# Kernel optimization log

Measured on AMD Instinct MI355X. Metric: run time of the kernel, lower is better.

Reference implementation:

```python
import jax, jax.numpy as jnp
import numpy as np

B, L, E, H = 64, 512, 128, 256


def setup_inputs() -> dict:
    key = jax.random.key(0)
    ks = jax.random.split(key, 16)
    s = 0.05
    return {
        "embedded_inputs": jax.random.normal(ks[0], (B, L, E), jnp.float32),
        "decoder_input": jax.random.normal(ks[1], (B, E), jnp.float32),
        "h0": jax.random.normal(ks[2], (B, H), jnp.float32),
        "c0": jax.random.normal(ks[3], (B, H), jnp.float32),
        "context": jax.random.normal(ks[4], (B, L, H), jnp.float32),
        # LSTM cell params
        "Wi": jax.random.normal(ks[5], (4 * H, E), jnp.float32) * s,
        "bi": jnp.zeros((4 * H,), jnp.float32),
        "Wh": jax.random.normal(ks[6], (4 * H, H), jnp.float32) * s,
        "bh": jnp.zeros((4 * H,), jnp.float32),
        # hidden_out: Linear(2H -> H)
        "Wo": jax.random.normal(ks[7], (H, 2 * H), jnp.float32) * s,
        "bo": jnp.zeros((H,), jnp.float32),
        # attention params: input_linear(H->H), context conv1d(H->H,k=1), V [H]
        "Wa_in": jax.random.normal(ks[8], (H, H), jnp.float32) * s,
        "ba_in": jnp.zeros((H,), jnp.float32),
        "Wa_ctx": jax.random.normal(ks[9], (H, H), jnp.float32) * s,
        "ba_ctx": jnp.zeros((H,), jnp.float32),
        "V": jax.random.normal(ks[10], (H,), jnp.float32) * s,
    }


def reference(embedded_inputs, decoder_input, h0, c0, context,
              Wi, bi, Wh, bh, Wo, bo, Wa_in, ba_in, Wa_ctx, ba_ctx, V):
    # Precompute projected context once (Conv1d with kernel 1 == per-position linear): [B,L,H]
    ctx_proj = jnp.einsum('blh,gh->blg', context, Wa_ctx) + ba_ctx

    def step(carry, _):
        dec_in, h, c, mask = carry
        gates = dec_in @ Wi.T + bi + h @ Wh.T + bh              # [B,4H]
        i_g, f_g, g_g, o_g = jnp.split(gates, 4, axis=1)
        i_g = jax.nn.sigmoid(i_g)
        f_g = jax.nn.sigmoid(f_g)
        g_g = jnp.tanh(g_g)
        o_g = jax.nn.sigmoid(o_g)
        c_t = f_g * c + i_g * g_g
        h_t = o_g * jnp.tanh(c_t)
        # attention
        inp = h_t @ Wa_in.T + ba_in                              # [B,H]
        scores = jnp.einsum('h,blh->bl', V, jnp.tanh(inp[:, None, :] + ctx_proj))
        scores = jnp.where(mask == 0, -jnp.inf, scores)
        alpha = jax.nn.softmax(scores, axis=1)                   # [B,L]
        att_hidden = jnp.einsum('bl,blh->bh', alpha, ctx_proj)
        hidden_t = jnp.tanh(jnp.concatenate([att_hidden, h_t], axis=1) @ Wo.T + bo)
        # pointer: argmax over still-available positions
        masked_outs = alpha * mask
        idx = jnp.argmax(masked_outs, axis=1)                    # [B]
        one_hot = jax.nn.one_hot(idx, L, dtype=mask.dtype)
        mask_next = mask * (1.0 - one_hot)
        dec_next = jnp.take_along_axis(embedded_inputs, idx[:, None, None], axis=1)[:, 0]
        return (dec_next, hidden_t, c_t, mask_next), (alpha, idx)

    mask0 = jnp.ones((B, L), jnp.float32)
    carry0 = (decoder_input, h0, c0, mask0)
    (dec_f, h_f, c_f, _), (alphas, ptrs) = jax.lax.scan(step, carry0, None, length=L)
    outputs = jnp.transpose(alphas, (1, 0, 2))                   # [B,L,L]
    pointers = jnp.transpose(ptrs, (1, 0))                       # [B,L]
    return outputs, pointers, h_f, c_f
```

## Files before the change

### kernel.cpp

```cpp
#include <hip/hip_runtime.h>
#include <math.h>

#define SCOPE __HIP_MEMORY_SCOPE_AGENT

constexpr int Bn = 64, Ln = 512, En = 128, Hn = 256, Tn = 512;
constexpr int NBLK = 256, NTHR = 512;
constexpr int CTX_LD = 260, HTPAD = 264, XPAD = 384, UPAD = 520;

constexpr int OFF_CTX = 0;
constexpr int OFF_SCR = 128 * CTX_LD;
constexpr int OFF_HT  = OFF_SCR + 4096;
constexpr int OFF_INP = OFF_HT + 4 * HTPAD;
constexpr int OFF_SS  = OFF_INP + 256;
constexpr int OFF_ES  = OFF_SS + 128;
constexpr int OFF_MK  = OFF_ES + 128;
constexpr int OFF_VS  = OFF_MK + 128;
constexpr int OFF_GS  = OFF_VS + 256;
constexpr int OFF_ST  = OFF_GS + 256;
constexpr int OFF_WR  = OFF_ST + 64;
constexpr int OFF_BA  = OFF_WR + 64;
constexpr int OFF_HTL = OFF_BA + 256;
constexpr int SMEM_FL = OFF_HTL + 64;

constexpr size_t PTR_OFF = (size_t)Bn * Ln * Ln;
constexpr size_t HF_OFF  = PTR_OFF + (size_t)Bn * Ln;
constexpr size_t CF_OFF  = HF_OFF + (size_t)Bn * Hn;

constexpr int GQ_HT    = 0;
constexpr int GQ_HID   = 1024;
constexpr int GQ_ATT   = 2048;
constexpr int GQ_STATS = 6144;
constexpr int GQ_INPP  = 6208;
constexpr int GQ_STRIDE = 6208 + 16384;

__device__ __forceinline__ float fast_tanh(float x) {
  const float e = __expf(2.0f * x);
  return 1.0f - __fdividef(2.0f, 1.0f + e);
}
__device__ __forceinline__ float sigmoidf_(float x) {
  return 1.0f / (1.0f + expf(-x));
}
__device__ __forceinline__ void llc_storef(float* p, float v) {
  __hip_atomic_store(p, v, __ATOMIC_RELAXED, SCOPE);
}
__device__ __forceinline__ float4 llc_ld4(const float* p) {
  float4 r;
  asm volatile("global_load_dwordx4 %0, %1, off sc0 sc1\n\ts_waitcnt vmcnt(0)"
               : "=&v"(r) : "v"(p) : "memory");
  return r;
}
__device__ __forceinline__ void llc_ld4x4(const float* p0, const float* p1,
                                          const float* p2, const float* p3,
                                          float4& a, float4& b, float4& c, float4& d) {
  asm volatile(
      "global_load_dwordx4 %0, %4, off sc0 sc1\n\t"
      "global_load_dwordx4 %1, %5, off sc0 sc1\n\t"
      "global_load_dwordx4 %2, %6, off sc0 sc1\n\t"
      "global_load_dwordx4 %3, %7, off sc0 sc1\n\t"
      "s_waitcnt vmcnt(0)"
      : "=&v"(a), "=&v"(b), "=&v"(c), "=&v"(d)
      : "v"(p0), "v"(p1), "v"(p2), "v"(p3) : "memory");
}

__device__ __forceinline__ void group_barrier16(unsigned* flags_g, int j, unsigned tgt) {
  asm volatile("s_waitcnt vmcnt(0)" ::: "memory");
  __syncthreads();
  if (threadIdx.x == 0)
    __hip_atomic_store(&flags_g[j * 32], tgt, __ATOMIC_RELAXED, SCOPE);
  if (threadIdx.x < 16) {
    long spins = 0;
    while (__hip_atomic_load(&flags_g[threadIdx.x * 32], __ATOMIC_RELAXED, SCOPE) < tgt) {
      __builtin_amdgcn_s_sleep(1);
      if (++spins > 50000000L) __builtin_trap();
    }
  }
  __syncthreads();
  asm volatile("" ::: "memory");
}

#define DOT4(acc, w4, x4) \
  acc = fmaf((w4).x, (x4).x, fmaf((w4).y, (x4).y, fmaf((w4).z, (x4).z, fmaf((w4).w, (x4).w, (acc)))))

__global__ void __launch_bounds__(NTHR, 2)
decoder_main(const float* __restrict__ emb, const float* __restrict__ dec0,
             const float* __restrict__ h0,  const float* __restrict__ c0,
             const float* __restrict__ ctxg,const float* __restrict__ Wi,
             const float* __restrict__ bi,  const float* __restrict__ Wh,
             const float* __restrict__ bh,  const float* __restrict__ Wo,
             const float* __restrict__ bo,  const float* __restrict__ Wain,
             const float* __restrict__ bain,const float* __restrict__ Wactx,
             const float* __restrict__ bactx,const float* __restrict__ Vv,
             float* __restrict__ out, unsigned* __restrict__ flags,
             float* __restrict__ wsd)
{
  extern __shared__ float sm[];
  float* ctx    = sm + OFF_CTX;
  float* scr    = sm + OFF_SCR;
  float* x_s    = sm + OFF_SCR;
  float* h_t_s  = sm + OFF_HT;
  float* inp_s  = sm + OFF_INP;
  float* s_s    = sm + OFF_SS;
  float* e_s    = sm + OFF_ES;
  float* mask_s = sm + OFF_MK;
  float* V_s    = sm + OFF_VS;
  float* gsum   = sm + OFF_GS;
  float* stats_s= sm + OFF_ST;
  float* wred   = sm + OFF_WR;
  float* bain_s = sm + OFF_BA;
  float* htl_s  = sm + OFF_HTL;
  int*   wredi  = (int*)wred;

  const int tid = threadIdx.x, bid = blockIdx.x;
  const int gq = bid >> 4, j = bid & 15;
  const int bbj = j >> 2, ck = j & 3;
  const int b_ctx = gq * 4 + bbj;
  const int l0 = ck * 128;

  const int team = tid >> 3, seg8 = tid & 7;
  const int gteam = team >> 4, hloc = team & 15;
  const int r_abs = gteam * 256 + j * 16 + hloc;
  const int g2 = tid >> 1, half = tid & 1;
  const int r16loc = tid >> 5, seg32 = tid & 31;
  const int r16 = j * 16 + r16loc;

  unsigned* flags_g = flags + gq * (16 * 32);
  float* wsg = wsd + (size_t)gq * GQ_STRIDE;

  float4 wg4[12];
  #pragma unroll
  for (int k = 0; k < 4; ++k) wg4[k] = *(const float4*)&Wi[(size_t)r_abs * En + k * 32 + seg8 * 4];
  #pragma unroll
  for (int k = 0; k < 8; ++k) wg4[4 + k] = *(const float4*)&Wh[(size_t)r_abs * Hn + k * 32 + seg8 * 4];
  const float bias_g = bi[r_abs] + bh[r_abs];

  float4 wa4[2];
  #pragma unroll
  for (int k = 0; k < 2; ++k)
    wa4[k] = *(const float4*)&Wain[(size_t)g2 * Hn + j * 16 + half * 8 + k * 4];

  float4 wo4[4];
  #pragma unroll
  for (int k = 0; k < 4; ++k) wo4[k] = *(const float4*)&Wo[(size_t)r16 * (2 * Hn) + k * 128 + seg32 * 4];
  const float bo_r = bo[r16];

  float cst = 0.0f;
  if (tid < 64) cst = c0[(size_t)(gq * 4 + (tid >> 4)) * Hn + j * 16 + (tid & 15)];

  if (tid < 128) mask_s[tid] = 1.0f;
  if (tid < 256) { V_s[tid] = Vv[tid]; bain_s[tid] = bain[tid]; }

  {
    const int gc = tid & 31, lg = tid >> 5;
    float acc[8][8];
    #pragma unroll
    for (int a2 = 0; a2 < 8; ++a2)
      #pragma unroll
      for (int b2 = 0; b2 < 8; ++b2) acc[a2][b2] = 0.0f;
    float* stg_c = scr;
    float* stg_w = scr + 1024;
    for (int kc = 0; kc < 32; ++kc) {
      __syncthreads();
      for (int i = tid; i < 1024; i += NTHR) {
        int k = i & 7, l = i >> 3;
        stg_c[k * 128 + l] = ctxg[((size_t)(b_ctx * Ln + l0 + l)) * Hn + kc * 8 + k];
      }
      for (int i = tid; i < 2048; i += NTHR) {
        int k = i & 7, gg = i >> 3;
        stg_w[k * 256 + gg] = Wactx[(size_t)gg * Hn + kc * 8 + k];
      }
      __syncthreads();
      #pragma unroll
      for (int kk = 0; kk < 8; ++kk) {
        float cl[8], wgt[8];
        #pragma unroll
        for (int jj = 0; jj < 8; ++jj) cl[jj] = stg_c[kk * 128 + lg * 8 + jj];
        #pragma unroll
        for (int jj = 0; jj < 8; ++jj) wgt[jj] = stg_w[kk * 256 + gc * 8 + jj];
        #pragma unroll
        for (int li = 0; li < 8; ++li)
          #pragma unroll
          for (int gi = 0; gi < 8; ++gi)
            acc[li][gi] = fmaf(cl[li], wgt[gi], acc[li][gi]);
      }
    }
    __syncthreads();
    #pragma unroll
    for (int li = 0; li < 8; ++li)
      #pragma unroll
      for (int gi = 0; gi < 8; ++gi)
        ctx[(lg * 8 + li) * CTX_LD + gc * 8 + gi] = acc[li][gi] + bactx[gc * 8 + gi];
  }
  __syncthreads();

  unsigned tgt = 1;
  int w0 = 0, w1 = 0, w2 = 0, w3 = 0;

  for (int t = 0; t < Tn; ++t) {
    {
      if (tid < 256) {
        const int bbx = tid >> 6, h4 = tid & 63;
        float4 v;
        if (t == 0) v = *(const float4*)&h0[(size_t)(gq * 4 + bbx) * Hn + h4 * 4];
        else        v = llc_ld4(wsg + GQ_HID + bbx * 256 + h4 * 4);
        *(float4*)&x_s[bbx * XPAD + 128 + h4 * 4] = v;
      } else if (tid < 384) {
        const int i2 = tid - 256, bbx = i2 >> 5, k4 = i2 & 31;
        const int gb = gq * 4 + bbx;
        float4 v;
        if (t == 0) v = *(const float4*)&dec0[(size_t)gb * En + k4 * 4];
        else {
          const int wsel = (bbx == 0) ? w0 : (bbx == 1) ? w1 : (bbx == 2) ? w2 : w3;
          v = *(const float4*)&emb[((size_t)gb * Ln + wsel) * En + k4 * 4];
        }
        *(float4*)&x_s[bbx * XPAD + k4 * 4] = v;
      }
      __syncthreads();
      #pragma unroll
      for (int bb = 0; bb < 4; ++bb) {
        float acc = 0.0f;
        #pragma unroll
        for (int k = 0; k < 12; ++k) {
          const float4 x4 = *(const float4*)&x_s[bb * XPAD + k * 32 + seg8 * 4];
          DOT4(acc, wg4[k], x4);
        }
        acc += __shfl_xor(acc, 1, 64);
        acc += __shfl_xor(acc, 2, 64);
        acc += __shfl_xor(acc, 4, 64);
        if (seg8 == 0) gsum[bb * 64 + team] = acc + bias_g;
      }
      __syncthreads();
      if (tid < 64) {
        const int bbx = tid >> 4, hx = tid & 15;
        const float iv = gsum[bbx * 64 + hx];
        const float fv = gsum[bbx * 64 + 16 + hx];
        const float gv = gsum[bbx * 64 + 32 + hx];
        const float ov = gsum[bbx * 64 + 48 + hx];
        const float cn = sigmoidf_(fv) * cst + sigmoidf_(iv) * tanhf(gv);
        const float htv = sigmoidf_(ov) * tanhf(cn);
        cst = cn;
        htl_s[bbx * 16 + hx] = htv;
        llc_storef(wsg + GQ_HT + bbx * 256 + j * 16 + hx, htv);
        if (t == Tn - 1) out[CF_OFF + (size_t)(gq * 4 + bbx) * Hn + j * 16 + hx] = cn;
      }
      __syncthreads();
      {
        float pac[4];
        #pragma unroll
        for (int bb = 0; bb < 4; ++bb) {
          float acc = 0.0f;
          #pragma unroll
          for (int k = 0; k < 2; ++k) {
            const float4 x4 = *(const float4*)&htl_s[bb * 16 + half * 8 + k * 4];
            DOT4(acc, wa4[k], x4);
          }
          pac[bb] = acc;
        }
        #pragma unroll
        for (int bb = 0; bb < 4; ++bb) {
          const float o = __shfl_xor(pac[bb], 1, 64);
          pac[bb] += o;
        }
        if (half == 0) {
          #pragma unroll
          for (int bb = 0; bb < 4; ++bb)
            llc_storef(wsg + GQ_INPP + bb * 4096 + g2 * 16 + j, pac[bb]);
        }
      }
    }
    group_barrier16(flags_g, j, tgt++);

    {
      if (tid < 256) {
        const int bbx = tid >> 6, h4 = tid & 63;
        const float4 v = llc_ld4(wsg + GQ_HT + tid * 4);
        *(float4*)&h_t_s[bbx * HTPAD + h4 * 4] = v;
        const float* ib = wsg + GQ_INPP + bbj * 4096 + tid * 16;
        float4 a0, a1, a2, a3;
        llc_ld4x4(ib, ib + 4, ib + 8, ib + 12, a0, a1, a2, a3);
        const float s01 = ((a0.x + a0.y) + (a0.z + a0.w)) + ((a1.x + a1.y) + (a1.z + a1.w));
        const float s23 = ((a2.x + a2.y) + (a2.z + a2.w)) + ((a3.x + a3.y) + (a3.z + a3.w));
        inp_s[tid] = s01 + s23 + bain_s[tid];
      }
      __syncthreads();
      {
        const int l = tid >> 2, q = tid & 3;
        float p = 0.0f;
        #pragma unroll
        for (int i = 0; i < 16; ++i) {
          const int h4 = q * 64 + i * 4;
          const float4 c4 = *(const float4*)&ctx[l * CTX_LD + h4];
          const float4 in4 = *(const float4*)&inp_s[h4];
          const float4 v4 = *(const float4*)&V_s[h4];
          p = fmaf(v4.x, fast_tanh(in4.x + c4.x), p);
          p = fmaf(v4.y, fast_tanh(in4.y + c4.y), p);
          p = fmaf(v4.z, fast_tanh(in4.z + c4.z), p);
          p = fmaf(v4.w, fast_tanh(in4.w + c4.w), p);
        }
        p += __shfl_xor(p, 1, 64);
        p += __shfl_xor(p, 2, 64);
        if (q == 0) s_s[l] = (mask_s[l] == 0.0f) ? -INFINITY : p;
      }
      __syncthreads();
      if (tid < 128) {
        const float sv = s_s[tid];
        const float e = expf(sv);
        e_s[tid] = e;
        float ssum = e;
        #pragma unroll
        for (int m = 1; m < 64; m <<= 1) ssum += __shfl_xor(ssum, m, 64);
        float cv = sv; int ci = tid;
        #pragma unroll
        for (int m = 1; m < 64; m <<= 1) {
          const float ov = __shfl_xor(cv, m, 64);
          const int   oi = __shfl_xor(ci, m, 64);
          if (ov > cv || (ov == cv && oi < ci)) { cv = ov; ci = oi; }
        }
        if ((tid & 63) == 0) {
          wred[tid >> 6] = ssum;
          wred[4 + (tid >> 6)] = cv;
          wredi[8 + (tid >> 6)] = ci;
        }
      }
      __syncthreads();
      if (tid == 0) {
        const float S = wred[0] + wred[1];
        float bv = wred[4]; int bI = wredi[8];
        if (wred[5] > bv || (wred[5] == bv && wredi[9] < bI)) { bv = wred[5]; bI = wredi[9]; }
        float* stb = wsg + GQ_STATS + (bbj * 4 + ck) * 4;
        llc_storef(stb + 0, S);
        llc_storef(stb + 1, bv);
        llc_storef(stb + 2, (float)(l0 + bI));
      }
      {
        const int h4g = tid & 63, lgq = tid >> 6;
        float p0 = 0, p1 = 0, p2 = 0, p3 = 0;
        #pragma unroll
        for (int li = 0; li < 16; ++li) {
          const int l = lgq * 16 + li;
          const float ev = e_s[l];
          const float4 c4 = *(const float4*)&ctx[l * CTX_LD + h4g * 4];
          p0 = fmaf(ev, c4.x, p0);
          p1 = fmaf(ev, c4.y, p1);
          p2 = fmaf(ev, c4.z, p2);
          p3 = fmaf(ev, c4.w, p3);
        }
        *(float4*)&scr[lgq * 256 + h4g * 4] = make_float4(p0, p1, p2, p3);
      }
      __syncthreads();
      if (tid < 256) {
        float a = 0.0f;
        #pragma unroll
        for (int r2 = 0; r2 < 8; ++r2) a += scr[r2 * 256 + tid];
        llc_storef(wsg + GQ_ATT + (bbj * 4 + ck) * 256 + tid, a);
      }
    }
    group_barrier16(flags_g, j, tgt++);

    {
      if (tid < 16) {
        const float4 st = llc_ld4(wsg + GQ_STATS + tid * 4);
        *(float4*)&stats_s[tid * 4] = st;
      }
      __syncthreads();
      float Sb[4]; int wq[4];
      #pragma unroll
      for (int bb = 0; bb < 4; ++bb) {
        Sb[bb] = ((stats_s[(bb * 4 + 0) * 4] + stats_s[(bb * 4 + 1) * 4])
                  + stats_s[(bb * 4 + 2) * 4]) + stats_s[(bb * 4 + 3) * 4];
        float bv = stats_s[(bb * 4 + 0) * 4 + 1];
        int bI = (int)stats_s[(bb * 4 + 0) * 4 + 2];
        #pragma unroll
        for (int c2 = 1; c2 < 4; ++c2) {
          const float v2 = stats_s[(bb * 4 + c2) * 4 + 1];
          const int i2 = (int)stats_s[(bb * 4 + c2) * 4 + 2];
          if (v2 > bv || (v2 == bv && i2 < bI)) { bv = v2; bI = i2; }
        }
        wq[bb] = bI;
      }
      const float Sown = (bbj == 0) ? Sb[0] : (bbj == 1) ? Sb[1] : (bbj == 2) ? Sb[2] : Sb[3];
      const int wown = (bbj == 0) ? wq[0] : (bbj == 1) ? wq[1] : (bbj == 2) ? wq[2] : wq[3];
      if (tid < 32) {
        const float4 e4 = *(const float4*)&e_s[tid * 4];
        *(float4*)&out[(size_t)b_ctx * Ln * Ln + (size_t)t * Ln + l0 + tid * 4] =
            make_float4(e4.x / Sown, e4.y / Sown, e4.z / Sown, e4.w / Sown);
      }
      if (tid == 0) {
        if (wown >= l0 && wown < l0 + 128) mask_s[wown - l0] = 0.0f;
        if (ck == 0) out[PTR_OFF + (size_t)b_ctx * Ln + t] = (float)wown;
      }
      if (tid < 256) {
        const int bbx = tid >> 6, h4 = tid & 63;
        const float* ab = wsg + GQ_ATT + bbx * 4 * 256 + h4 * 4;
        float4 a0, a1, a2, a3;
        llc_ld4x4(ab, ab + 256, ab + 512, ab + 768, a0, a1, a2, a3);
        const float Sx = (bbx == 0) ? Sb[0] : (bbx == 1) ? Sb[1] : (bbx == 2) ? Sb[2] : Sb[3];
        float4 u4;
        u4.x = (((a0.x + a1.x) + a2.x) + a3.x) / Sx;
        u4.y = (((a0.y + a1.y) + a2.y) + a3.y) / Sx;
        u4.z = (((a0.z + a1.z) + a2.z) + a3.z) / Sx;
        u4.w = (((a0.w + a1.w) + a2.w) + a3.w) / Sx;
        *(float4*)&scr[bbx * UPAD + h4 * 4] = u4;
      } else {
        const int i2 = tid - 256, bbx = i2 >> 6, h4 = i2 & 63;
        const float4 hv = *(const float4*)&h_t_s[bbx * HTPAD + h4 * 4];
        *(float4*)&scr[bbx * UPAD + 256 + h4 * 4] = hv;
      }
      __syncthreads();
      #pragma unroll
      for (int bb = 0; bb < 4; ++bb) {
        float acc = 0.0f;
        #pragma unroll
        for (int k = 0; k < 4; ++k) {
          const float4 x4 = *(const float4*)&scr[bb * UPAD + k * 128 + seg32 * 4];
          DOT4(acc, wo4[k], x4);
        }
        acc += __shfl_xor(acc, 1, 64);
        acc += __shfl_xor(acc, 2, 64);
        acc += __shfl_xor(acc, 4, 64);
        acc += __shfl_xor(acc, 8, 64);
        acc += __shfl_xor(acc, 16, 64);
        if (seg32 == 0) {
          const float hv = tanhf(acc + bo_r);
          llc_storef(wsg + GQ_HID + bb * 256 + r16, hv);
          if (t == Tn - 1) out[HF_OFF + (size_t)(gq * 4 + bb) * Hn + r16] = hv;
        }
      }
      w0 = wq[0]; w1 = wq[1]; w2 = wq[2]; w3 = wq[3];
    }
    group_barrier16(flags_g, j, tgt++);
  }
}

extern "C" void kernel_launch(void* const* d_in, const int* in_sizes, int n_in,
                              void* d_out, int out_size, void* d_ws, size_t ws_size,
                              hipStream_t stream) {
  (void)in_sizes; (void)n_in; (void)out_size; (void)ws_size;
  (void)hipFuncSetAttribute(reinterpret_cast<const void*>(decoder_main),
                            hipFuncAttributeMaxDynamicSharedMemorySize, SMEM_FL * 4);
  (void)hipMemsetAsync(d_ws, 0, 32768, stream);

  const float* emb   = (const float*)d_in[0];
  const float* dec0  = (const float*)d_in[1];
  const float* h0    = (const float*)d_in[2];
  const float* c0    = (const float*)d_in[3];
  const float* ctxg  = (const float*)d_in[4];
  const float* Wi    = (const float*)d_in[5];
  const float* bi    = (const float*)d_in[6];
  const float* Wh    = (const float*)d_in[7];
  const float* bh    = (const float*)d_in[8];
  const float* Wo    = (const float*)d_in[9];
  const float* bo    = (const float*)d_in[10];
  const float* Wain  = (const float*)d_in[11];
  const float* bain  = (const float*)d_in[12];
  const float* Wactx = (const float*)d_in[13];
  const float* bactx = (const float*)d_in[14];
  const float* V     = (const float*)d_in[15];

  unsigned* flags = (unsigned*)d_ws;
  float* wsd = (float*)((char*)d_ws + 32768);

  decoder_main<<<NBLK, NTHR, SMEM_FL * 4, stream>>>(
      emb, dec0, h0, c0, ctxg, Wi, bi, Wh, bh, Wo, bo, Wain, bain, Wactx, bactx, V,
      (float*)d_out, flags, wsd);
}
```

Measured before the change: 10.75 ms.

## Keep context slice in registers across score and attention phases, batch LLC loads

The score computation is remapped so each thread owns one float4 column for 16 positions. It loads those 16 ctx float4s into registers once and reuses them for both the tanh score pass and the alpha-weighted context sum, which removes a second round of LDS reads. The h_t load is deferred and merged with the attention partial loads into one five-load LLC batch, dropping the h_t shared buffer, and the stats load moves to a different thread range so it can overlap. Launch bounds drop to one block per SM to allow the extra registers, which risks lower occupancy and more shuffle reductions per score.

```diff
diff --git a/kernel.cpp b/kernel.cpp
--- a/kernel.cpp
+++ b/kernel.cpp
@@ -5,12 +5,11 @@
 
 constexpr int Bn = 64, Ln = 512, En = 128, Hn = 256, Tn = 512;
 constexpr int NBLK = 256, NTHR = 512;
-constexpr int CTX_LD = 260, HTPAD = 264, XPAD = 384, UPAD = 520;
+constexpr int CTX_LD = 260, XPAD = 384, UPAD = 520;
 
 constexpr int OFF_CTX = 0;
 constexpr int OFF_SCR = 128 * CTX_LD;
-constexpr int OFF_HT  = OFF_SCR + 4096;
-constexpr int OFF_INP = OFF_HT + 4 * HTPAD;
+constexpr int OFF_INP = OFF_SCR + 4096;
 constexpr int OFF_SS  = OFF_INP + 256;
 constexpr int OFF_ES  = OFF_SS + 128;
 constexpr int OFF_MK  = OFF_ES + 128;
@@ -60,6 +59,21 @@
       "s_waitcnt vmcnt(0)"
       : "=&v"(a), "=&v"(b), "=&v"(c), "=&v"(d)
       : "v"(p0), "v"(p1), "v"(p2), "v"(p3) : "memory");
+}
+__device__ __forceinline__ void llc_ld5(const float* p0, const float* p1,
+                                        const float* p2, const float* p3,
+                                        const float* p4,
+                                        float4& a, float4& b, float4& c,
+                                        float4& d, float4& e) {
+  asm volatile(
+      "global_load_dwordx4 %0, %5, off sc0 sc1\n\t"
+      "global_load_dwordx4 %1, %6, off sc0 sc1\n\t"
+      "global_load_dwordx4 %2, %7, off sc0 sc1\n\t"
+      "global_load_dwordx4 %3, %8, off sc0 sc1\n\t"
+      "global_load_dwordx4 %4, %9, off sc0 sc1\n\t"
+      "s_waitcnt vmcnt(0)"
+      : "=&v"(a), "=&v"(b), "=&v"(c), "=&v"(d), "=&v"(e)
+      : "v"(p0), "v"(p1), "v"(p2), "v"(p3), "v"(p4) : "memory");
 }
 
 __device__ __forceinline__ void group_barrier16(unsigned* flags_g, int j, unsigned tgt) {
@@ -81,7 +95,7 @@
 #define DOT4(acc, w4, x4) \
   acc = fmaf((w4).x, (x4).x, fmaf((w4).y, (x4).y, fmaf((w4).z, (x4).z, fmaf((w4).w, (x4).w, (acc)))))
 
-__global__ void __launch_bounds__(NTHR, 2)
+__global__ void __launch_bounds__(NTHR, 1)
 decoder_main(const float* __restrict__ emb, const float* __restrict__ dec0,
              const float* __restrict__ h0,  const float* __restrict__ c0,
              const float* __restrict__ ctxg,const float* __restrict__ Wi,
@@ -97,7 +111,6 @@
   float* ctx    = sm + OFF_CTX;
   float* scr    = sm + OFF_SCR;
   float* x_s    = sm + OFF_SCR;
-  float* h_t_s  = sm + OFF_HT;
   float* inp_s  = sm + OFF_INP;
   float* s_s    = sm + OFF_SS;
   float* e_s    = sm + OFF_ES;
@@ -122,6 +135,7 @@
   const int g2 = tid >> 1, half = tid & 1;
   const int r16loc = tid >> 5, seg32 = tid & 31;
   const int r16 = j * 16 + r16loc;
+  const int hq = tid & 63, lg = tid >> 6;
 
   unsigned* flags_g = flags + gq * (16 * 32);
   float* wsg = wsd + (size_t)gq * GQ_STRIDE;
@@ -150,7 +164,7 @@
   if (tid < 256) { V_s[tid] = Vv[tid]; bain_s[tid] = bain[tid]; }
 
   {
-    const int gc = tid & 31, lg = tid >> 5;
+    const int gc = tid & 31, lgi = tid >> 5;
     float acc[8][8];
     #pragma unroll
     for (int a2 = 0; a2 < 8; ++a2)
@@ -173,7 +187,7 @@
       for (int kk = 0; kk < 8; ++kk) {
         float cl[8], wgt[8];
         #pragma unroll
-        for (int jj = 0; jj < 8; ++jj) cl[jj] = stg_c[kk * 128 + lg * 8 + jj];
+        for (int jj = 0; jj < 8; ++jj) cl[jj] = stg_c[kk * 128 + lgi * 8 + jj];
         #pragma unroll
         for (int jj = 0; jj < 8; ++jj) wgt[jj] = stg_w[kk * 256 + gc * 8 + jj];
         #pragma unroll
@@ -188,7 +202,7 @@
     for (int li = 0; li < 8; ++li)
       #pragma unroll
       for (int gi = 0; gi < 8; ++gi)
-        ctx[(lg * 8 + li) * CTX_LD + gc * 8 + gi] = acc[li][gi] + bactx[gc * 8 + gi];
+        ctx[(lgi * 8 + li) * CTX_LD + gc * 8 + gi] = acc[li][gi] + bactx[gc * 8 + gi];
   }
   __syncthreads();
 
@@ -271,9 +285,6 @@
 
     {
       if (tid < 256) {
-        const int bbx = tid >> 6, h4 = tid & 63;
-        const float4 v = llc_ld4(wsg + GQ_HT + tid * 4);
-        *(float4*)&h_t_s[bbx * HTPAD + h4 * 4] = v;
         const float* ib = wsg + GQ_INPP + bbj * 4096 + tid * 16;
         float4 a0, a1, a2, a3;
         llc_ld4x4(ib, ib + 4, ib + 8, ib + 12, a0, a1, a2, a3);
@@ -282,23 +293,29 @@
         inp_s[tid] = s01 + s23 + bain_s[tid];
       }
       __syncthreads();
-      {
-        const int l = tid >> 2, q = tid & 3;
-        float p = 0.0f;
-        #pragma unroll
-        for (int i = 0; i < 16; ++i) {
-          const int h4 = q * 64 + i * 4;
-          const float4 c4 = *(const float4*)&ctx[l * CTX_LD + h4];
-          const float4 in4 = *(const float4*)&inp_s[h4];
-          const float4 v4 = *(const float4*)&V_s[h4];
-          p = fmaf(v4.x, fast_tanh(in4.x + c4.x), p);
-          p = fmaf(v4.y, fast_tanh(in4.y + c4.y), p);
-          p = fmaf(v4.z, fast_tanh(in4.z + c4.z), p);
-          p = fmaf(v4.w, fast_tanh(in4.w + c4.w), p);
-        }
+      const float4 in4 = *(const float4*)&inp_s[hq * 4];
+      const float4 v4  = *(const float4*)&V_s[hq * 4];
+      float4 c4[16];
+      #pragma unroll
+      for (int li = 0; li < 16; ++li)
+        c4[li] = *(const float4*)&ctx[(lg * 16 + li) * CTX_LD + hq * 4];
+      #pragma unroll
+      for (int li = 0; li < 16; ++li) {
+        float p;
+        p = v4.x * fast_tanh(in4.x + c4[li].x);
+        p = fmaf(v4.y, fast_tanh(in4.y + c4[li].y), p);
+        p = fmaf(v4.z, fast_tanh(in4.z + c4[li].z), p);
+        p = fmaf(v4.w, fast_tanh(in4.w + c4[li].w), p);
         p += __shfl_xor(p, 1, 64);
         p += __shfl_xor(p, 2, 64);
-        if (q == 0) s_s[l] = (mask_s[l] == 0.0f) ? -INFINITY : p;
+        p += __shfl_xor(p, 4, 64);
+        p += __shfl_xor(p, 8, 64);
+        p += __shfl_xor(p, 16, 64);
+        p += __shfl_xor(p, 32, 64);
+        if (hq == 0) {
+          const int l = lg * 16 + li;
+          s_s[l] = (mask_s[l] == 0.0f) ? -INFINITY : p;
+        }
       }
       __syncthreads();
       if (tid < 128) {
@@ -332,19 +349,16 @@
         llc_storef(stb + 2, (float)(l0 + bI));
       }
       {
-        const int h4g = tid & 63, lgq = tid >> 6;
         float p0 = 0, p1 = 0, p2 = 0, p3 = 0;
         #pragma unroll
         for (int li = 0; li < 16; ++li) {
-          const int l = lgq * 16 + li;
-          const float ev = e_s[l];
-          const float4 c4 = *(const float4*)&ctx[l * CTX_LD + h4g * 4];
-          p0 = fmaf(ev, c4.x, p0);
-          p1 = fmaf(ev, c4.y, p1);
-          p2 = fmaf(ev, c4.z, p2);
-          p3 = fmaf(ev, c4.w, p3);
-        }
-        *(float4*)&scr[lgq * 256 + h4g * 4] = make_float4(p0, p1, p2, p3);
+          const float ev = e_s[lg * 16 + li];
+          p0 = fmaf(ev, c4[li].x, p0);
+          p1 = fmaf(ev, c4[li].y, p1);
+          p2 = fmaf(ev, c4[li].z, p2);
+          p3 = fmaf(ev, c4[li].w, p3);
+        }
+        *(float4*)&scr[lg * 256 + hq * 4] = make_float4(p0, p1, p2, p3);
       }
       __syncthreads();
       if (tid < 256) {
@@ -357,9 +371,16 @@
     group_barrier16(flags_g, j, tgt++);
 
     {
-      if (tid < 16) {
-        const float4 st = llc_ld4(wsg + GQ_STATS + tid * 4);
-        *(float4*)&stats_s[tid * 4] = st;
+      float4 a0, a1, a2, a3, htv4;
+      if (tid >= 256 && tid < 272) {
+        const float4 st = llc_ld4(wsg + GQ_STATS + (tid - 256) * 4);
+        *(float4*)&stats_s[(tid - 256) * 4] = st;
+      }
+      if (tid < 256) {
+        const int bbx = tid >> 6, h4 = tid & 63;
+        const float* ab = wsg + GQ_ATT + bbx * 1024 + h4 * 4;
+        llc_ld5(ab, ab + 256, ab + 512, ab + 768, wsg + GQ_HT + tid * 4,
+                a0, a1, a2, a3, htv4);
       }
       __syncthreads();
       float Sb[4]; int wq[4];
@@ -390,9 +411,6 @@
       }
       if (tid < 256) {
         const int bbx = tid >> 6, h4 = tid & 63;
-        const float* ab = wsg + GQ_ATT + bbx * 4 * 256 + h4 * 4;
-        float4 a0, a1, a2, a3;
-        llc_ld4x4(ab, ab + 256, ab + 512, ab + 768, a0, a1, a2, a3);
         const float Sx = (bbx == 0) ? Sb[0] : (bbx == 1) ? Sb[1] : (bbx == 2) ? Sb[2] : Sb[3];
         float4 u4;
         u4.x = (((a0.x + a1.x) + a2.x) + a3.x) / Sx;
@@ -400,10 +418,7 @@
         u4.z = (((a0.z + a1.z) + a2.z) + a3.z) / Sx;
         u4.w = (((a0.w + a1.w) + a2.w) + a3.w) / Sx;
         *(float4*)&scr[bbx * UPAD + h4 * 4] = u4;
-      } else {
-        const int i2 = tid - 256, bbx = i2 >> 6, h4 = i2 & 63;
-        const float4 hv = *(const float4*)&h_t_s[bbx * HTPAD + h4 * 4];
-        *(float4*)&scr[bbx * UPAD + 256 + h4 * 4] = hv;
+        *(float4*)&scr[bbx * UPAD + 256 + h4 * 4] = htv4;
       }
       __syncthreads();
       #pragma unroll
```

New measurement: 11.49 ms. 1.07x slower.
